# Optimization experiments

Hardware: AMD Instinct MI355X
Metric: run time of the kernel (lower is better)

The kernel has to match this reference:

```python
import jax, jax.numpy as jnp
import numpy as np

K_IN = 9      # input_patch_size
K_OUT = 3     # output_patch_size
C_IN = 4      # nb_of_input_features
C_OUT = 2     # nb_of_output_features
HID = 50      # int_layer_width
B, H, W = 16, 128, 128
CUT = K_IN // 2 - K_OUT // 2  # border pixels cut from output (3)


def _unfold(x, k):
    # x: [B, C, H, W] -> [B, C*k*k, L] with torch unfold ordering (c, ki, kj)
    b, c, h, w = x.shape
    ho, wo = h - k + 1, w - k + 1
    cols = jnp.stack([x[:, :, i:i + ho, j:j + wo]
                      for i in range(k) for j in range(k)], axis=2)  # [B,C,k*k,ho,wo]
    return cols.reshape(b, c * k * k, ho * wo)


def _fold_add(patches, oh, ow):
    # patches: [B, C, k, k, ho, wo] -> overlap-add into [B, C, oh, ow]
    b, c, k, _, ho, wo = patches.shape
    out = jnp.zeros((b, c, oh, ow), dtype=patches.dtype)
    for i in range(k):
        for j in range(k):
            out = out.at[:, :, i:i + ho, j:j + wo].add(patches[:, :, i, j])
    return out


def setup_inputs() -> dict:
    key = jax.random.key(0)
    ks = jax.random.split(key, 7)
    f_in = C_IN * K_IN * K_IN      # 324
    f_out = C_OUT * K_OUT * K_OUT  # 18
    s1 = 1.0 / np.sqrt(f_in)
    s2 = 1.0 / np.sqrt(HID)
    return {
        "x": jax.random.normal(ks[0], (B, C_IN, H, W), dtype=jnp.float32),
        "W1": jax.random.uniform(ks[1], (f_in, HID), jnp.float32, -s1, s1),
        "b1": jax.random.uniform(ks[2], (HID,), jnp.float32, -s1, s1),
        "W2": jax.random.uniform(ks[3], (HID, HID), jnp.float32, -s2, s2),
        "b2": jax.random.uniform(ks[4], (HID,), jnp.float32, -s2, s2),
        "W3": jax.random.uniform(ks[5], (HID, f_out), jnp.float32, -s2, s2),
        "b3": jax.random.uniform(ks[6], (f_out,), jnp.float32, -s2, s2),
    }


def reference(x, W1, b1, W2, b2, W3, b3):
    b, c, h, w = x.shape
    oh, ow = h - 2 * CUT, w - 2 * CUT          # 122, 122
    ho, wo = h - K_IN + 1, w - K_IN + 1        # 120, 120 (= oh-K_OUT+1)
    # unfold -> [B, L, C_in*K_in^2] -> flatten rows
    cols = _unfold(x, K_IN)                    # [B, 324, L]
    feats = cols.transpose(0, 2, 1).reshape(b * ho * wo, -1)
    # 3-layer MLP
    hmid = jax.nn.relu(feats @ W1 + b1)
    hmid = jax.nn.relu(hmid @ W2 + b2)
    out = hmid @ W3 + b3                       # [B*L, C_out*K_out^2]
    # fold (overlap-add), torch feature ordering (c, ki, kj)
    patches = out.reshape(b, ho, wo, C_OUT, K_OUT, K_OUT)
    patches = patches.transpose(0, 3, 4, 5, 1, 2)  # [B, C_out, k, k, ho, wo]
    res = _fold_add(patches, oh, ow)
    # divisor = fold(unfold(ones)) -> per-pixel overlap count
    ones_patches = jnp.ones((1, 1, K_OUT, K_OUT, ho, wo), dtype=x.dtype)
    divisor = _fold_add(ones_patches, oh, ow)  # [1,1,oh,ow]
    return res / divisor
```

## Files before the change

### kernel.cpp

```cpp
#include <hip/hip_runtime.h>
#include <hip/hip_bf16.h>

#define BATCH   16
#define C_INF   4
#define H_IN    128
#define W_IN    128
#define HID     50
#define F_OUT   18
#define HO      120
#define WO      120
#define OH      122
#define OW      122
#define NPOS    (BATCH * HO * WO)
#define MBLK    128
#define NBLKS   (NPOS / MBLK)

#define NB1     (11*4*2*64*8)
#define NB2     (2*4*2*64*8)
#define NB3     (2*2*2*64*8)
#define NWF     (NB1 + NB2 + NB3)
#define NXP     (BATCH*C_INF*H_IN*W_IN)
#define WOFF    (NPOS * F_OUT)

typedef float  v4f    __attribute__((ext_vector_type(4)));
typedef short  short8 __attribute__((ext_vector_type(8)));
typedef __bf16 v8bf   __attribute__((ext_vector_type(8)));
typedef int    v4i    __attribute__((ext_vector_type(4)));
typedef uint   u32x4  __attribute__((ext_vector_type(4)));
typedef u32x4  u32x4_a4 __attribute__((aligned(4)));

__device__ inline short f2bf_hi(float x) {
    __hip_bfloat16 h = __float2bfloat16(x);
    return __builtin_bit_cast(short, h);
}
__device__ inline float bf2f(short s) {
    __hip_bfloat16 h = __builtin_bit_cast(__hip_bfloat16, s);
    return __bfloat162float(h);
}
__device__ inline uint hipair(uint a, uint b) { return __builtin_amdgcn_perm(b, a, 0x07060302u); }
__device__ inline uint lopair(uint a, uint b) { return __builtin_amdgcn_perm(b, a, 0x05040100u); }

__device__ inline int slot_to_k1(int s, int qb, int e) {
    if (s < 9) {
        int pair = s*4 + qb;
        int c = pair/9, ki = pair - c*9;
        return c*81 + ki*9 + e;
    }
    int r = (s-9)*32 + qb*8 + e;
    if (r >= 36) return -1;
    int c = r/9, ki = r - c*9;
    return c*81 + ki*9 + 8;
}

__global__ __launch_bounds__(256)
void prep_kernel(const float* __restrict__ x,
                 const float* __restrict__ W1, const float* __restrict__ W2,
                 const float* __restrict__ W3,
                 uint* __restrict__ xp, short* __restrict__ wf)
{
    int i = blockIdx.x * 256 + threadIdx.x;
    if (i < NXP) {
        float v = x[i];
        short hi = f2bf_hi(v);
        short lo = f2bf_hi(v - bf2f(hi));
        xp[i] = ((uint)(ushort)hi << 16) | (uint)(ushort)lo;
        return;
    }
    i -= NXP;
    if (i >= NWF) return;
    float val;
    int p;
    if (i < NB1) {
        int t = i;
        int e = t & 7, lane = (t >> 3) & 63; p = (t >> 9) & 1;
        int rest = t >> 10;
        int u = rest & 3, s = rest >> 2;
        int k = slot_to_k1(s, lane >> 4, e);
        int n = u*16 + (lane & 15);
        val = (k >= 0 && n < HID) ? W1[k*HID + n] : 0.f;
    } else if (i < NB1 + NB2) {
        int t = i - NB1;
        int e = t & 7, lane = (t >> 3) & 63; p = (t >> 9) & 1;
        int rest = t >> 10;
        int u = rest & 3, s = rest >> 2;
        int k = s*32 + ((lane >> 4) << 3) + e;
        int n = u*16 + (lane & 15);
        val = (k < HID && n < HID) ? W2[k*HID + n] : 0.f;
    } else {
        int t = i - NB1 - NB2;
        int e = t & 7, lane = (t >> 3) & 63; p = (t >> 9) & 1;
        int rest = t >> 10;
        int u = rest & 1, s = rest >> 1;
        int k = s*32 + ((lane >> 4) << 3) + e;
        int n = u*16 + (lane & 15);
        val = (k < HID && n < F_OUT) ? W3[k*F_OUT + n] : 0.f;
    }
    short hi = f2bf_hi(val);
    wf[i] = (p == 0) ? hi : f2bf_hi(val - bf2f(hi));
}

__global__ __launch_bounds__(256, 4)
void mfma_mlp(const uint* __restrict__ xp,
              const float* __restrict__ b1, const float* __restrict__ b2,
              const float* __restrict__ b3,
              const short* __restrict__ wf, float* __restrict__ out3)
{
    __shared__ short h_hi[128 * 72];
    __shared__ short h_lo[128 * 72];

    const int tid  = threadIdx.x;
    const int lane = tid & 63;
    const int w    = tid >> 6;
    const int wm   = w >> 1, wn = w & 1;
    const int q    = lane >> 4, col = lane & 15;
    const int mbase = blockIdx.x * MBLK;

    int xbase[4];
    #pragma unroll
    for (int t = 0; t < 4; ++t) {
        int pos = mbase + wm*64 + t*16 + col;
        int b   = pos / (HO*WO); int rem = pos - b*(HO*WO);
        int y   = rem / WO;      int xc  = rem - y*WO;
        xbase[t] = b*(C_INF*H_IN*W_IN) + y*W_IN + xc;
    }

    const v4i* B1 = (const v4i*)wf;
    const v4i* B2 = (const v4i*)(wf + NB1);
    const v4i* B3 = (const v4i*)(wf + NB1 + NB2);

    v4f acc[4][2];
    #pragma unroll
    for (int t = 0; t < 4; ++t)
        #pragma unroll
        for (int u = 0; u < 2; ++u)
            acc[t][u] = (v4f){0.f, 0.f, 0.f, 0.f};

    #pragma unroll 3
    for (int s = 0; s < 9; ++s) {
        const int pair = s*4 + q;
        const int c = pair/9, ki = pair - c*9;
        const int off = c*(H_IN*W_IN) + ki*W_IN;

        v4i bhv[2], blv[2];
        #pragma unroll
        for (int uu = 0; uu < 2; ++uu) {
            int u  = 2*wn + uu;
            int fb = ((s*4 + u)*2)*64 + lane;
            bhv[uu] = B1[fb];
            blv[uu] = B1[fb + 64];
        }

        u32x4 wa[4], wb[4];
        #pragma unroll
        for (int t = 0; t < 4; ++t) {
            const uint* p = &xp[xbase[t] + off];
            wa[t] = *(const u32x4_a4*)(p);
            wb[t] = *(const u32x4_a4*)(p + 4);
        }
        short8 ah[4], al[4];
        #pragma unroll
        for (int t = 0; t < 4; ++t) {
            u32x4 hh, ll;
            hh.x = hipair(wa[t].x, wa[t].y); hh.y = hipair(wa[t].z, wa[t].w);
            hh.z = hipair(wb[t].x, wb[t].y); hh.w = hipair(wb[t].z, wb[t].w);
            ll.x = lopair(wa[t].x, wa[t].y); ll.y = lopair(wa[t].z, wa[t].w);
            ll.z = lopair(wb[t].x, wb[t].y); ll.w = lopair(wb[t].z, wb[t].w);
            ah[t] = __builtin_bit_cast(short8, hh);
            al[t] = __builtin_bit_cast(short8, ll);
        }
        #pragma unroll
        for (int uu = 0; uu < 2; ++uu) {
            v8bf bh = __builtin_bit_cast(v8bf, bhv[uu]);
            v8bf bl = __builtin_bit_cast(v8bf, blv[uu]);
            #pragma unroll
            for (int t = 0; t < 4; ++t) {
                v8bf a_h = __builtin_bit_cast(v8bf, ah[t]);
                v8bf a_l = __builtin_bit_cast(v8bf, al[t]);
                acc[t][uu] = __builtin_amdgcn_mfma_f32_16x16x32_bf16(a_h, bh, acc[t][uu], 0, 0, 0);
                acc[t][uu] = __builtin_amdgcn_mfma_f32_16x16x32_bf16(a_l, bh, acc[t][uu], 0, 0, 0);
                acc[t][uu] = __builtin_amdgcn_mfma_f32_16x16x32_bf16(a_h, bl, acc[t][uu], 0, 0, 0);
            }
        }
    }
    #pragma unroll
    for (int sr = 0; sr < 2; ++sr) {
        const int s = 9 + sr;
        short8 ah[4], al[4];
        #pragma unroll
        for (int e = 0; e < 8; ++e) {
            int r = sr*32 + q*8 + e;
            bool valid = (r < 36);
            int c = valid ? r/9 : 0;
            int ki = r - c*9;
            int off = c*(H_IN*W_IN) + ki*W_IN + 8;
            #pragma unroll
            for (int t = 0; t < 4; ++t) {
                uint wv = valid ? xp[xbase[t] + off] : 0u;
                ah[t][e] = (short)(wv >> 16);
                al[t][e] = (short)(wv & 0xffffu);
            }
        }
        #pragma unroll
        for (int uu = 0; uu < 2; ++uu) {
            int u  = 2*wn + uu;
            int fb = ((s*4 + u)*2)*64 + lane;
            v8bf bh = __builtin_bit_cast(v8bf, B1[fb]);
            v8bf bl = __builtin_bit_cast(v8bf, B1[fb + 64]);
            #pragma unroll
            for (int t = 0; t < 4; ++t) {
                v8bf a_h = __builtin_bit_cast(v8bf, ah[t]);
                v8bf a_l = __builtin_bit_cast(v8bf, al[t]);
                acc[t][uu] = __builtin_amdgcn_mfma_f32_16x16x32_bf16(a_h, bh, acc[t][uu], 0, 0, 0);
                acc[t][uu] = __builtin_amdgcn_mfma_f32_16x16x32_bf16(a_l, bh, acc[t][uu], 0, 0, 0);
                acc[t][uu] = __builtin_amdgcn_mfma_f32_16x16x32_bf16(a_h, bl, acc[t][uu], 0, 0, 0);
            }
        }
    }

    #pragma unroll
    for (int uu = 0; uu < 2; ++uu) {
        int j = (2*wn + uu)*16 + col;
        float bias = (j < HID) ? b1[j] : 0.f;
        #pragma unroll
        for (int t = 0; t < 4; ++t) {
            #pragma unroll
            for (int r = 0; r < 4; ++r) {
                float v = fmaxf(acc[t][uu][r] + bias, 0.f);
                int m = wm*64 + t*16 + q*4 + r;
                short hi = f2bf_hi(v);
                h_hi[m*72 + j] = hi;
                h_lo[m*72 + j] = f2bf_hi(v - bf2f(hi));
            }
        }
    }
    __syncthreads();

    v4f acc2[4][2];
    #pragma unroll
    for (int t = 0; t < 4; ++t)
        #pragma unroll
        for (int u = 0; u < 2; ++u)
            acc2[t][u] = (v4f){0.f, 0.f, 0.f, 0.f};

    #pragma unroll
    for (int s = 0; s < 2; ++s) {
        short8 ah2[4], al2[4];
        #pragma unroll
        for (int t = 0; t < 4; ++t) {
            int m = wm*64 + t*16 + col;
            ah2[t] = *(const short8*)&h_hi[m*72 + s*32 + q*8];
            al2[t] = *(const short8*)&h_lo[m*72 + s*32 + q*8];
        }
        #pragma unroll
        for (int uu = 0; uu < 2; ++uu) {
            int u  = 2*wn + uu;
            int fb = ((s*4 + u)*2)*64 + lane;
            v8bf bh = __builtin_bit_cast(v8bf, B2[fb]);
            v8bf bl = __builtin_bit_cast(v8bf, B2[fb + 64]);
            #pragma unroll
            for (int t = 0; t < 4; ++t) {
                v8bf a_h = __builtin_bit_cast(v8bf, ah2[t]);
                v8bf a_l = __builtin_bit_cast(v8bf, al2[t]);
                acc2[t][uu] = __builtin_amdgcn_mfma_f32_16x16x32_bf16(a_h, bh, acc2[t][uu], 0, 0, 0);
                acc2[t][uu] = __builtin_amdgcn_mfma_f32_16x16x32_bf16(a_l, bh, acc2[t][uu], 0, 0, 0);
                acc2[t][uu] = __builtin_amdgcn_mfma_f32_16x16x32_bf16(a_h, bl, acc2[t][uu], 0, 0, 0);
            }
        }
    }
    __syncthreads();

    #pragma unroll
    for (int uu = 0; uu < 2; ++uu) {
        int j = (2*wn + uu)*16 + col;
        float bias = (j < HID) ? b2[j] : 0.f;
        #pragma unroll
        for (int t = 0; t < 4; ++t) {
            #pragma unroll
            for (int r = 0; r < 4; ++r) {
                float v = fmaxf(acc2[t][uu][r] + bias, 0.f);
                int m = wm*64 + t*16 + q*4 + r;
                short hi = f2bf_hi(v);
                h_hi[m*72 + j] = hi;
                h_lo[m*72 + j] = f2bf_hi(v - bf2f(hi));
            }
        }
    }
    __syncthreads();

    v4f acc3[4];
    #pragma unroll
    for (int t = 0; t < 4; ++t) acc3[t] = (v4f){0.f, 0.f, 0.f, 0.f};

    #pragma unroll
    for (int s = 0; s < 2; ++s) {
        short8 ah3[4], al3[4];
        #pragma unroll
        for (int t = 0; t < 4; ++t) {
            int m = wm*64 + t*16 + col;
            ah3[t] = *(const short8*)&h_hi[m*72 + s*32 + q*8];
            al3[t] = *(const short8*)&h_lo[m*72 + s*32 + q*8];
        }
        int fb = ((s*2 + wn)*2)*64 + lane;
        v8bf bh = __builtin_bit_cast(v8bf, B3[fb]);
        v8bf bl = __builtin_bit_cast(v8bf, B3[fb + 64]);
        #pragma unroll
        for (int t = 0; t < 4; ++t) {
            v8bf a_h = __builtin_bit_cast(v8bf, ah3[t]);
            v8bf a_l = __builtin_bit_cast(v8bf, al3[t]);
            acc3[t] = __builtin_amdgcn_mfma_f32_16x16x32_bf16(a_h, bh, acc3[t], 0, 0, 0);
            acc3[t] = __builtin_amdgcn_mfma_f32_16x16x32_bf16(a_l, bh, acc3[t], 0, 0, 0);
            acc3[t] = __builtin_amdgcn_mfma_f32_16x16x32_bf16(a_h, bl, acc3[t], 0, 0, 0);
        }
    }
    __syncthreads();

    float* ot = (float*)h_hi;
    {
        int j = wn*16 + col;
        if (j < F_OUT) {
            float bias = b3[j];
            #pragma unroll
            for (int t = 0; t < 4; ++t) {
                #pragma unroll
                for (int r = 0; r < 4; ++r) {
                    int m = wm*64 + t*16 + q*4 + r;
                    ot[j*129 + m] = acc3[t][r] + bias;
                }
            }
        }
    }
    __syncthreads();
    for (int i = tid; i < F_OUT * 128; i += 256) {
        int j2 = i >> 7, m2 = i & 127;
        out3[j2*NPOS + mbase + m2] = ot[j2*129 + m2];
    }
}

__global__ __launch_bounds__(256)
void fold_kernel(const float* __restrict__ out3, float* __restrict__ out)
{
    const int idx = blockIdx.x * 256 + threadIdx.x;
    const int total = BATCH * 2 * OH * OW;
    if (idx >= total) return;

    int t = idx;
    const int ox = t % OW; t /= OW;
    const int oy = t % OH; t /= OH;
    const int c  = t & 1;  t >>= 1;
    const int b  = t;

    const int ylo = max(0, oy - 2), yhi = min(HO - 1, oy);
    const int xlo = max(0, ox - 2), xhi = min(WO - 1, ox);

    float s = 0.f;
    for (int y = ylo; y <= yhi; ++y) {
        const int ki = oy - y;
        for (int xx = xlo; xx <= xhi; ++xx) {
            const int kj = ox - xx;
            const int o  = (c*3 + ki)*3 + kj;
            s += out3[o*NPOS + (b*HO + y)*WO + xx];
        }
    }
    const float div = (float)((yhi - ylo + 1) * (xhi - xlo + 1));
    out[idx] = s / div;
}

extern "C" void kernel_launch(void* const* d_in, const int* in_sizes, int n_in,
                              void* d_out, int out_size, void* d_ws, size_t ws_size,
                              hipStream_t stream)
{
    const float* x  = (const float*)d_in[0];
    const float* W1 = (const float*)d_in[1];
    const float* b1 = (const float*)d_in[2];
    const float* W2 = (const float*)d_in[3];
    const float* b2 = (const float*)d_in[4];
    const float* W3 = (const float*)d_in[5];
    const float* b3 = (const float*)d_in[6];

    float* out3 = (float*)d_ws;
    short* wf   = (short*)d_ws + 2*(size_t)WOFF;
    uint*  xp   = (uint*)((char*)d_ws + (size_t)WOFF*4 + (size_t)NWF*2);

    const int nprep = (NXP + NWF + 255) / 256;
    prep_kernel<<<nprep, 256, 0, stream>>>(x, W1, W2, W3, xp, wf);

    mfma_mlp<<<NBLKS, 256, 0, stream>>>(xp, b1, b2, b3, wf, out3);

    const int total = BATCH * 2 * OH * OW;
    fold_kernel<<<(total + 255) / 256, 256, 0, stream>>>(out3, (float*)d_out);
}
```

Measured before the change: 124.7 us.

## Fuse fold into MLP epilogue via atomics and drop lo-split of hidden activations

```diff
diff --git a/kernel.cpp b/kernel.cpp
--- a/kernel.cpp
+++ b/kernel.cpp
@@ -20,7 +20,6 @@
 #define NB3     (2*2*2*64*8)
 #define NWF     (NB1 + NB2 + NB3)
 #define NXP     (BATCH*C_INF*H_IN*W_IN)
-#define WOFF    (NPOS * F_OUT)
 
 typedef float  v4f    __attribute__((ext_vector_type(4)));
 typedef short  short8 __attribute__((ext_vector_type(8)));
@@ -103,10 +102,9 @@
 void mfma_mlp(const uint* __restrict__ xp,
               const float* __restrict__ b1, const float* __restrict__ b2,
               const float* __restrict__ b3,
-              const short* __restrict__ wf, float* __restrict__ out3)
+              const short* __restrict__ wf, float* __restrict__ out)
 {
     __shared__ short h_hi[128 * 72];
-    __shared__ short h_lo[128 * 72];
 
     const int tid  = threadIdx.x;
     const int lane = tid & 63;
@@ -227,9 +225,7 @@
             for (int r = 0; r < 4; ++r) {
                 float v = fmaxf(acc[t][uu][r] + bias, 0.f);
                 int m = wm*64 + t*16 + q*4 + r;
-                short hi = f2bf_hi(v);
-                h_hi[m*72 + j] = hi;
-                h_lo[m*72 + j] = f2bf_hi(v - bf2f(hi));
+                h_hi[m*72 + j] = f2bf_hi(v);
             }
         }
     }
@@ -244,12 +240,11 @@
 
     #pragma unroll
     for (int s = 0; s < 2; ++s) {
-        short8 ah2[4], al2[4];
+        short8 ah2[4];
         #pragma unroll
         for (int t = 0; t < 4; ++t) {
             int m = wm*64 + t*16 + col;
             ah2[t] = *(const short8*)&h_hi[m*72 + s*32 + q*8];
-            al2[t] = *(const short8*)&h_lo[m*72 + s*32 + q*8];
         }
         #pragma unroll
         for (int uu = 0; uu < 2; ++uu) {
@@ -260,9 +255,7 @@
             #pragma unroll
             for (int t = 0; t < 4; ++t) {
                 v8bf a_h = __builtin_bit_cast(v8bf, ah2[t]);
-                v8bf a_l = __builtin_bit_cast(v8bf, al2[t]);
                 acc2[t][uu] = __builtin_amdgcn_mfma_f32_16x16x32_bf16(a_h, bh, acc2[t][uu], 0, 0, 0);
-                acc2[t][uu] = __builtin_amdgcn_mfma_f32_16x16x32_bf16(a_l, bh, acc2[t][uu], 0, 0, 0);
                 acc2[t][uu] = __builtin_amdgcn_mfma_f32_16x16x32_bf16(a_h, bl, acc2[t][uu], 0, 0, 0);
             }
         }
@@ -279,9 +272,7 @@
             for (int r = 0; r < 4; ++r) {
                 float v = fmaxf(acc2[t][uu][r] + bias, 0.f);
                 int m = wm*64 + t*16 + q*4 + r;
-                short hi = f2bf_hi(v);
-                h_hi[m*72 + j] = hi;
-                h_lo[m*72 + j] = f2bf_hi(v - bf2f(hi));
+                h_hi[m*72 + j] = f2bf_hi(v);
             }
         }
     }
@@ -293,12 +284,11 @@
 
     #pragma unroll
     for (int s = 0; s < 2; ++s) {
-        short8 ah3[4], al3[4];
+        short8 ah3[4];
         #pragma unroll
         for (int t = 0; t < 4; ++t) {
             int m = wm*64 + t*16 + col;
             ah3[t] = *(const short8*)&h_hi[m*72 + s*32 + q*8];
-            al3[t] = *(const short8*)&h_lo[m*72 + s*32 + q*8];
         }
         int fb = ((s*2 + wn)*2)*64 + lane;
         v8bf bh = __builtin_bit_cast(v8bf, B3[fb]);
@@ -306,63 +296,33 @@
         #pragma unroll
         for (int t = 0; t < 4; ++t) {
             v8bf a_h = __builtin_bit_cast(v8bf, ah3[t]);
-            v8bf a_l = __builtin_bit_cast(v8bf, al3[t]);
             acc3[t] = __builtin_amdgcn_mfma_f32_16x16x32_bf16(a_h, bh, acc3[t], 0, 0, 0);
-            acc3[t] = __builtin_amdgcn_mfma_f32_16x16x32_bf16(a_l, bh, acc3[t], 0, 0, 0);
             acc3[t] = __builtin_amdgcn_mfma_f32_16x16x32_bf16(a_h, bl, acc3[t], 0, 0, 0);
         }
     }
-    __syncthreads();
-
-    float* ot = (float*)h_hi;
-    {
-        int j = wn*16 + col;
-        if (j < F_OUT) {
-            float bias = b3[j];
-            #pragma unroll
-            for (int t = 0; t < 4; ++t) {
-                #pragma unroll
-                for (int r = 0; r < 4; ++r) {
-                    int m = wm*64 + t*16 + q*4 + r;
-                    ot[j*129 + m] = acc3[t][r] + bias;
-                }
-            }
-        }
-    }
-    __syncthreads();
-    for (int i = tid; i < F_OUT * 128; i += 256) {
-        int j2 = i >> 7, m2 = i & 127;
-        out3[j2*NPOS + mbase + m2] = ot[j2*129 + m2];
-    }
-}
-
-__global__ __launch_bounds__(256)
-void fold_kernel(const float* __restrict__ out3, float* __restrict__ out)
-{
-    const int idx = blockIdx.x * 256 + threadIdx.x;
-    const int total = BATCH * 2 * OH * OW;
-    if (idx >= total) return;
-
-    int t = idx;
-    const int ox = t % OW; t /= OW;
-    const int oy = t % OH; t /= OH;
-    const int c  = t & 1;  t >>= 1;
-    const int b  = t;
-
-    const int ylo = max(0, oy - 2), yhi = min(HO - 1, oy);
-    const int xlo = max(0, ox - 2), xhi = min(WO - 1, ox);
-
-    float s = 0.f;
-    for (int y = ylo; y <= yhi; ++y) {
-        const int ki = oy - y;
-        for (int xx = xlo; xx <= xhi; ++xx) {
-            const int kj = ox - xx;
-            const int o  = (c*3 + ki)*3 + kj;
-            s += out3[o*NPOS + (b*HO + y)*WO + xx];
-        }
-    }
-    const float div = (float)((yhi - ylo + 1) * (xhi - xlo + 1));
-    out[idx] = s / div;
+
+    int j = wn*16 + col;
+    if (j < F_OUT) {
+        const float bias = b3[j];
+        const int c  = j / 9, r9 = j - c*9;
+        const int ki = r9 / 3, kj = r9 - ki*3;
+        #pragma unroll
+        for (int t = 0; t < 4; ++t) {
+            #pragma unroll
+            for (int r = 0; r < 4; ++r) {
+                int pos = mbase + wm*64 + t*16 + q*4 + r;
+                int b   = pos / (HO*WO); int rem = pos - b*(HO*WO);
+                int y   = rem / WO;      int xc  = rem - y*WO;
+                int oy  = y + ki, ox = xc + kj;
+                int cy  = min(HO-1, oy) - max(0, oy-2) + 1;
+                int cx  = min(WO-1, ox) - max(0, ox-2) + 1;
+                float sy = (cy == 3) ? (1.f/3.f) : ((cy == 2) ? 0.5f : 1.f);
+                float sx = (cx == 3) ? (1.f/3.f) : ((cx == 2) ? 0.5f : 1.f);
+                float v  = (acc3[t][r] + bias) * (sy * sx);
+                atomicAdd(&out[((b*2 + c)*OH + oy)*OW + ox], v);
+            }
+        }
+    }
 }
 
 extern "C" void kernel_launch(void* const* d_in, const int* in_sizes, int n_in,
@@ -377,15 +337,13 @@
     const float* W3 = (const float*)d_in[5];
     const float* b3 = (const float*)d_in[6];
 
-    float* out3 = (float*)d_ws;
-    short* wf   = (short*)d_ws + 2*(size_t)WOFF;
-    uint*  xp   = (uint*)((char*)d_ws + (size_t)WOFF*4 + (size_t)NWF*2);
+    uint*  xp = (uint*)d_ws;
+    short* wf = (short*)(xp + NXP);
+
+    hipMemsetAsync(d_out, 0, (size_t)out_size * sizeof(float), stream);
 
     const int nprep = (NXP + NWF + 255) / 256;
     prep_kernel<<<nprep, 256, 0, stream>>>(x, W1, W2, W3, xp, wf);
 
-    mfma_mlp<<<NBLKS, 256, 0, stream>>>(xp, b1, b2, b3, wf, out3);
-
-    const int total = BATCH * 2 * OH * OW;
-    fold_kernel<<<(total + 255) / 256, 256, 0, stream>>>(out3, (float*)d_out);
-}
+    mfma_mlp<<<NBLKS, 256, 0, stream>>>(xp, b1, b2, b3, wf, (float*)d_out);
+}
```

Measured after the change: 138.0 us. 10.6% more time.

## Fuse prep, MLP and fold into one persistent kernel with grid barriers

Applied to the files above, without the earlier changes.

```diff
diff --git a/kernel.cpp b/kernel.cpp
--- a/kernel.cpp
+++ b/kernel.cpp
@@ -14,6 +14,7 @@
 #define NPOS    (BATCH * HO * WO)
 #define MBLK    128
 #define NBLKS   (NPOS / MBLK)
+#define NB      512
 
 #define NB1     (11*4*2*64*8)
 #define NB2     (2*4*2*64*8)
@@ -21,6 +22,7 @@
 #define NWF     (NB1 + NB2 + NB3)
 #define NXP     (BATCH*C_INF*H_IN*W_IN)
 #define WOFF    (NPOS * F_OUT)
+#define NOUT    (BATCH * 2 * OH * OW)
 
 typedef float  v4f    __attribute__((ext_vector_type(4)));
 typedef short  short8 __attribute__((ext_vector_type(8)));
@@ -52,317 +54,323 @@
     return c*81 + ki*9 + 8;
 }
 
-__global__ __launch_bounds__(256)
-void prep_kernel(const float* __restrict__ x,
-                 const float* __restrict__ W1, const float* __restrict__ W2,
-                 const float* __restrict__ W3,
-                 uint* __restrict__ xp, short* __restrict__ wf)
-{
-    int i = blockIdx.x * 256 + threadIdx.x;
-    if (i < NXP) {
-        float v = x[i];
-        short hi = f2bf_hi(v);
-        short lo = f2bf_hi(v - bf2f(hi));
-        xp[i] = ((uint)(ushort)hi << 16) | (uint)(ushort)lo;
-        return;
-    }
-    i -= NXP;
-    if (i >= NWF) return;
-    float val;
-    int p;
-    if (i < NB1) {
-        int t = i;
-        int e = t & 7, lane = (t >> 3) & 63; p = (t >> 9) & 1;
-        int rest = t >> 10;
-        int u = rest & 3, s = rest >> 2;
-        int k = slot_to_k1(s, lane >> 4, e);
-        int n = u*16 + (lane & 15);
-        val = (k >= 0 && n < HID) ? W1[k*HID + n] : 0.f;
-    } else if (i < NB1 + NB2) {
-        int t = i - NB1;
-        int e = t & 7, lane = (t >> 3) & 63; p = (t >> 9) & 1;
-        int rest = t >> 10;
-        int u = rest & 3, s = rest >> 2;
-        int k = s*32 + ((lane >> 4) << 3) + e;
-        int n = u*16 + (lane & 15);
-        val = (k < HID && n < HID) ? W2[k*HID + n] : 0.f;
-    } else {
-        int t = i - NB1 - NB2;
-        int e = t & 7, lane = (t >> 3) & 63; p = (t >> 9) & 1;
-        int rest = t >> 10;
-        int u = rest & 1, s = rest >> 1;
-        int k = s*32 + ((lane >> 4) << 3) + e;
-        int n = u*16 + (lane & 15);
-        val = (k < HID && n < F_OUT) ? W3[k*F_OUT + n] : 0.f;
-    }
-    short hi = f2bf_hi(val);
-    wf[i] = (p == 0) ? hi : f2bf_hi(val - bf2f(hi));
-}
-
-__global__ __launch_bounds__(256, 4)
-void mfma_mlp(const uint* __restrict__ xp,
-              const float* __restrict__ b1, const float* __restrict__ b2,
-              const float* __restrict__ b3,
-              const short* __restrict__ wf, float* __restrict__ out3)
+__device__ inline void gbar(uint* flags, uint tag) {
+    __threadfence();
+    __syncthreads();
+    if (threadIdx.x == 0)
+        __hip_atomic_store(&flags[blockIdx.x], tag, __ATOMIC_RELEASE, __HIP_MEMORY_SCOPE_AGENT);
+    for (int f = (int)threadIdx.x; f < NB; f += 256) {
+        while (__hip_atomic_load(&flags[f], __ATOMIC_ACQUIRE, __HIP_MEMORY_SCOPE_AGENT) != tag)
+            __builtin_amdgcn_s_sleep(2);
+    }
+    __syncthreads();
+    __threadfence();
+}
+
+__global__ __launch_bounds__(256, 2)
+void fused_kernel(const float* __restrict__ x,
+                  const float* __restrict__ W1, const float* __restrict__ b1,
+                  const float* __restrict__ W2, const float* __restrict__ b2,
+                  const float* __restrict__ W3, const float* __restrict__ b3,
+                  float* __restrict__ out3, short* __restrict__ wf,
+                  uint* __restrict__ xp, uint* flags1, uint* flags2,
+                  float* __restrict__ out)
 {
     __shared__ short h_hi[128 * 72];
-    __shared__ short h_lo[128 * 72];
 
     const int tid  = threadIdx.x;
+    const int bid  = blockIdx.x;
+
+    if (tid == 0) {
+        __hip_atomic_store(&flags1[bid], 0u, __ATOMIC_RELAXED, __HIP_MEMORY_SCOPE_AGENT);
+        __hip_atomic_store(&flags2[bid], 0u, __ATOMIC_RELAXED, __HIP_MEMORY_SCOPE_AGENT);
+    }
+
+    for (int gi = bid*256 + tid; gi < NXP + NWF; gi += NB*256) {
+        if (gi < NXP) {
+            float v = x[gi];
+            short hi = f2bf_hi(v);
+            short lo = f2bf_hi(v - bf2f(hi));
+            xp[gi] = ((uint)(ushort)hi << 16) | (uint)(ushort)lo;
+        } else {
+            int i = gi - NXP;
+            float val; int p;
+            if (i < NB1) {
+                int t = i;
+                int e = t & 7, lane = (t >> 3) & 63; p = (t >> 9) & 1;
+                int rest = t >> 10;
+                int u = rest & 3, s = rest >> 2;
+                int k = slot_to_k1(s, lane >> 4, e);
+                int n = u*16 + (lane & 15);
+                val = (k >= 0 && n < HID) ? W1[k*HID + n] : 0.f;
+            } else if (i < NB1 + NB2) {
+                int t = i - NB1;
+                int e = t & 7, lane = (t >> 3) & 63; p = (t >> 9) & 1;
+                int rest = t >> 10;
+                int u = rest & 3, s = rest >> 2;
+                int k = s*32 + ((lane >> 4) << 3) + e;
+                int n = u*16 + (lane & 15);
+                val = (k < HID && n < HID) ? W2[k*HID + n] : 0.f;
+            } else {
+                int t = i - NB1 - NB2;
+                int e = t & 7, lane = (t >> 3) & 63; p = (t >> 9) & 1;
+                int rest = t >> 10;
+                int u = rest & 1, s = rest >> 1;
+                int k = s*32 + ((lane >> 4) << 3) + e;
+                int n = u*16 + (lane & 15);
+                val = (k < HID && n < F_OUT) ? W3[k*F_OUT + n] : 0.f;
+            }
+            short hi = f2bf_hi(val);
+            wf[i] = (p == 0) ? hi : f2bf_hi(val - bf2f(hi));
+        }
+    }
+
+    gbar(flags1, 1u);
+
     const int lane = tid & 63;
     const int w    = tid >> 6;
     const int wm   = w >> 1, wn = w & 1;
     const int q    = lane >> 4, col = lane & 15;
-    const int mbase = blockIdx.x * MBLK;
-
-    int xbase[4];
-    #pragma unroll
-    for (int t = 0; t < 4; ++t) {
-        int pos = mbase + wm*64 + t*16 + col;
-        int b   = pos / (HO*WO); int rem = pos - b*(HO*WO);
-        int y   = rem / WO;      int xc  = rem - y*WO;
-        xbase[t] = b*(C_INF*H_IN*W_IN) + y*W_IN + xc;
-    }
 
     const v4i* B1 = (const v4i*)wf;
     const v4i* B2 = (const v4i*)(wf + NB1);
     const v4i* B3 = (const v4i*)(wf + NB1 + NB2);
 
-    v4f acc[4][2];
-    #pragma unroll
-    for (int t = 0; t < 4; ++t)
-        #pragma unroll
-        for (int u = 0; u < 2; ++u)
-            acc[t][u] = (v4f){0.f, 0.f, 0.f, 0.f};
-
-    #pragma unroll 3
-    for (int s = 0; s < 9; ++s) {
-        const int pair = s*4 + q;
-        const int c = pair/9, ki = pair - c*9;
-        const int off = c*(H_IN*W_IN) + ki*W_IN;
-
-        v4i bhv[2], blv[2];
+    for (int unit = bid; unit < NBLKS; unit += NB) {
+        const int mbase = unit * MBLK;
+
+        int xbase[4];
+        #pragma unroll
+        for (int t = 0; t < 4; ++t) {
+            int pos = mbase + wm*64 + t*16 + col;
+            int b   = pos / (HO*WO); int rem = pos - b*(HO*WO);
+            int y   = rem / WO;      int xc  = rem - y*WO;
+            xbase[t] = b*(C_INF*H_IN*W_IN) + y*W_IN + xc;
+        }
+
+        v4f acc[4][2];
+        #pragma unroll
+        for (int t = 0; t < 4; ++t)
+            #pragma unroll
+            for (int u = 0; u < 2; ++u)
+                acc[t][u] = (v4f){0.f, 0.f, 0.f, 0.f};
+
+        #pragma unroll 3
+        for (int s = 0; s < 9; ++s) {
+            const int pair = s*4 + q;
+            const int c = pair/9, ki = pair - c*9;
+            const int off = c*(H_IN*W_IN) + ki*W_IN;
+
+            v4i bhv[2], blv[2];
+            #pragma unroll
+            for (int uu = 0; uu < 2; ++uu) {
+                int u  = 2*wn + uu;
+                int fb = ((s*4 + u)*2)*64 + lane;
+                bhv[uu] = B1[fb];
+                blv[uu] = B1[fb + 64];
+            }
+
+            u32x4 wa[4], wb[4];
+            #pragma unroll
+            for (int t = 0; t < 4; ++t) {
+                const uint* p = &xp[xbase[t] + off];
+                wa[t] = *(const u32x4_a4*)(p);
+                wb[t] = *(const u32x4_a4*)(p + 4);
+            }
+            short8 ah[4], al[4];
+            #pragma unroll
+            for (int t = 0; t < 4; ++t) {
+                u32x4 hh, ll;
+                hh.x = hipair(wa[t].x, wa[t].y); hh.y = hipair(wa[t].z, wa[t].w);
+                hh.z = hipair(wb[t].x, wb[t].y); hh.w = hipair(wb[t].z, wb[t].w);
+                ll.x = lopair(wa[t].x, wa[t].y); ll.y = lopair(wa[t].z, wa[t].w);
+                ll.z = lopair(wb[t].x, wb[t].y); ll.w = lopair(wb[t].z, wb[t].w);
+                ah[t] = __builtin_bit_cast(short8, hh);
+                al[t] = __builtin_bit_cast(short8, ll);
+            }
+            #pragma unroll
+            for (int uu = 0; uu < 2; ++uu) {
+                v8bf bh = __builtin_bit_cast(v8bf, bhv[uu]);
+                v8bf bl = __builtin_bit_cast(v8bf, blv[uu]);
+                #pragma unroll
+                for (int t = 0; t < 4; ++t) {
+                    v8bf a_h = __builtin_bit_cast(v8bf, ah[t]);
+                    v8bf a_l = __builtin_bit_cast(v8bf, al[t]);
+                    acc[t][uu] = __builtin_amdgcn_mfma_f32_16x16x32_bf16(a_h, bh, acc[t][uu], 0, 0, 0);
+                    acc[t][uu] = __builtin_amdgcn_mfma_f32_16x16x32_bf16(a_l, bh, acc[t][uu], 0, 0, 0);
+                    acc[t][uu] = __builtin_amdgcn_mfma_f32_16x16x32_bf16(a_h, bl, acc[t][uu], 0, 0, 0);
+                }
+            }
+        }
+        #pragma unroll
+        for (int sr = 0; sr < 2; ++sr) {
+            const int s = 9 + sr;
+            short8 ah[4], al[4];
+            #pragma unroll
+            for (int e = 0; e < 8; ++e) {
+                int r = sr*32 + q*8 + e;
+                bool valid = (r < 36);
+                int c = valid ? r/9 : 0;
+                int ki = r - c*9;
+                int off = c*(H_IN*W_IN) + ki*W_IN + 8;
+                #pragma unroll
+                for (int t = 0; t < 4; ++t) {
+                    uint wv = valid ? xp[xbase[t] + off] : 0u;
+                    ah[t][e] = (short)(wv >> 16);
+                    al[t][e] = (short)(wv & 0xffffu);
+                }
+            }
+            #pragma unroll
+            for (int uu = 0; uu < 2; ++uu) {
+                int u  = 2*wn + uu;
+                int fb = ((s*4 + u)*2)*64 + lane;
+                v8bf bh = __builtin_bit_cast(v8bf, B1[fb]);
+                v8bf bl = __builtin_bit_cast(v8bf, B1[fb + 64]);
+                #pragma unroll
+                for (int t = 0; t < 4; ++t) {
+                    v8bf a_h = __builtin_bit_cast(v8bf, ah[t]);
+                    v8bf a_l = __builtin_bit_cast(v8bf, al[t]);
+                    acc[t][uu] = __builtin_amdgcn_mfma_f32_16x16x32_bf16(a_h, bh, acc[t][uu], 0, 0, 0);
+                    acc[t][uu] = __builtin_amdgcn_mfma_f32_16x16x32_bf16(a_l, bh, acc[t][uu], 0, 0, 0);
+                    acc[t][uu] = __builtin_amdgcn_mfma_f32_16x16x32_bf16(a_h, bl, acc[t][uu], 0, 0, 0);
+                }
+            }
+        }
+
         #pragma unroll
         for (int uu = 0; uu < 2; ++uu) {
-            int u  = 2*wn + uu;
-            int fb = ((s*4 + u)*2)*64 + lane;
-            bhv[uu] = B1[fb];
-            blv[uu] = B1[fb + 64];
-        }
-
-        u32x4 wa[4], wb[4];
-        #pragma unroll
-        for (int t = 0; t < 4; ++t) {
-            const uint* p = &xp[xbase[t] + off];
-            wa[t] = *(const u32x4_a4*)(p);
-            wb[t] = *(const u32x4_a4*)(p + 4);
-        }
-        short8 ah[4], al[4];
-        #pragma unroll
-        for (int t = 0; t < 4; ++t) {
-            u32x4 hh, ll;
-            hh.x = hipair(wa[t].x, wa[t].y); hh.y = hipair(wa[t].z, wa[t].w);
-            hh.z = hipair(wb[t].x, wb[t].y); hh.w = hipair(wb[t].z, wb[t].w);
-            ll.x = lopair(wa[t].x, wa[t].y); ll.y = lopair(wa[t].z, wa[t].w);
-            ll.z = lopair(wb[t].x, wb[t].y); ll.w = lopair(wb[t].z, wb[t].w);
-            ah[t] = __builtin_bit_cast(short8, hh);
-            al[t] = __builtin_bit_cast(short8, ll);
-        }
+            int j = (2*wn + uu)*16 + col;
+            float bias = (j < HID) ? b1[j] : 0.f;
+            #pragma unroll
+            for (int t = 0; t < 4; ++t) {
+                #pragma unroll
+                for (int r = 0; r < 4; ++r) {
+                    float v = fmaxf(acc[t][uu][r] + bias, 0.f);
+                    int m = wm*64 + t*16 + q*4 + r;
+                    h_hi[m*72 + j] = f2bf_hi(v);
+                }
+            }
+        }
+        __syncthreads();
+
+        v4f acc2[4][2];
+        #pragma unroll
+        for (int t = 0; t < 4; ++t)
+            #pragma unroll
+            for (int u = 0; u < 2; ++u)
+                acc2[t][u] = (v4f){0.f, 0.f, 0.f, 0.f};
+
+        #pragma unroll
+        for (int s = 0; s < 2; ++s) {
+            short8 ah2[4];
+            #pragma unroll
+            for (int t = 0; t < 4; ++t) {
+                int m = wm*64 + t*16 + col;
+                ah2[t] = *(const short8*)&h_hi[m*72 + s*32 + q*8];
+            }
+            #pragma unroll
+            for (int uu = 0; uu < 2; ++uu) {
+                int u  = 2*wn + uu;
+                int fb = ((s*4 + u)*2)*64 + lane;
+                v8bf bh = __builtin_bit_cast(v8bf, B2[fb]);
+                v8bf bl = __builtin_bit_cast(v8bf, B2[fb + 64]);
+                #pragma unroll
+                for (int t = 0; t < 4; ++t) {
+                    v8bf a_h = __builtin_bit_cast(v8bf, ah2[t]);
+                    acc2[t][uu] = __builtin_amdgcn_mfma_f32_16x16x32_bf16(a_h, bh, acc2[t][uu], 0, 0, 0);
+                    acc2[t][uu] = __builtin_amdgcn_mfma_f32_16x16x32_bf16(a_h, bl, acc2[t][uu], 0, 0, 0);
+                }
+            }
+        }
+        __syncthreads();
+
         #pragma unroll
         for (int uu = 0; uu < 2; ++uu) {
-            v8bf bh = __builtin_bit_cast(v8bf, bhv[uu]);
-            v8bf bl = __builtin_bit_cast(v8bf, blv[uu]);
-            #pragma unroll
-            for (int t = 0; t < 4; ++t) {
-                v8bf a_h = __builtin_bit_cast(v8bf, ah[t]);
-                v8bf a_l = __builtin_bit_cast(v8bf, al[t]);
-                acc[t][uu] = __builtin_amdgcn_mfma_f32_16x16x32_bf16(a_h, bh, acc[t][uu], 0, 0, 0);
-                acc[t][uu] = __builtin_amdgcn_mfma_f32_16x16x32_bf16(a_l, bh, acc[t][uu], 0, 0, 0);
-                acc[t][uu] = __builtin_amdgcn_mfma_f32_16x16x32_bf16(a_h, bl, acc[t][uu], 0, 0, 0);
-            }
-        }
-    }
-    #pragma unroll
-    for (int sr = 0; sr < 2; ++sr) {
-        const int s = 9 + sr;
-        short8 ah[4], al[4];
-        #pragma unroll
-        for (int e = 0; e < 8; ++e) {
-            int r = sr*32 + q*8 + e;
-            bool valid = (r < 36);
-            int c = valid ? r/9 : 0;
-            int ki = r - c*9;
-            int off = c*(H_IN*W_IN) + ki*W_IN + 8;
-            #pragma unroll
-            for (int t = 0; t < 4; ++t) {
-                uint wv = valid ? xp[xbase[t] + off] : 0u;
-                ah[t][e] = (short)(wv >> 16);
-                al[t][e] = (short)(wv & 0xffffu);
-            }
-        }
-        #pragma unroll
-        for (int uu = 0; uu < 2; ++uu) {
-            int u  = 2*wn + uu;
-            int fb = ((s*4 + u)*2)*64 + lane;
-            v8bf bh = __builtin_bit_cast(v8bf, B1[fb]);
-            v8bf bl = __builtin_bit_cast(v8bf, B1[fb + 64]);
-            #pragma unroll
-            for (int t = 0; t < 4; ++t) {
-                v8bf a_h = __builtin_bit_cast(v8bf, ah[t]);
-                v8bf a_l = __builtin_bit_cast(v8bf, al[t]);
-                acc[t][uu] = __builtin_amdgcn_mfma_f32_16x16x32_bf16(a_h, bh, acc[t][uu], 0, 0, 0);
-                acc[t][uu] = __builtin_amdgcn_mfma_f32_16x16x32_bf16(a_l, bh, acc[t][uu], 0, 0, 0);
-                acc[t][uu] = __builtin_amdgcn_mfma_f32_16x16x32_bf16(a_h, bl, acc[t][uu], 0, 0, 0);
-            }
-        }
-    }
-
-    #pragma unroll
-    for (int uu = 0; uu < 2; ++uu) {
-        int j = (2*wn + uu)*16 + col;
-        float bias = (j < HID) ? b1[j] : 0.f;
-        #pragma unroll
-        for (int t = 0; t < 4; ++t) {
-            #pragma unroll
-            for (int r = 0; r < 4; ++r) {
-                float v = fmaxf(acc[t][uu][r] + bias, 0.f);
-                int m = wm*64 + t*16 + q*4 + r;
-                short hi = f2bf_hi(v);
-                h_hi[m*72 + j] = hi;
-                h_lo[m*72 + j] = f2bf_hi(v - bf2f(hi));
-            }
-        }
-    }
-    __syncthreads();
-
-    v4f acc2[4][2];
-    #pragma unroll
-    for (int t = 0; t < 4; ++t)
-        #pragma unroll
-        for (int u = 0; u < 2; ++u)
-            acc2[t][u] = (v4f){0.f, 0.f, 0.f, 0.f};
-
-    #pragma unroll
-    for (int s = 0; s < 2; ++s) {
-        short8 ah2[4], al2[4];
-        #pragma unroll
-        for (int t = 0; t < 4; ++t) {
-            int m = wm*64 + t*16 + col;
-            ah2[t] = *(const short8*)&h_hi[m*72 + s*32 + q*8];
-            al2[t] = *(const short8*)&h_lo[m*72 + s*32 + q*8];
-        }
-        #pragma unroll
-        for (int uu = 0; uu < 2; ++uu) {
-            int u  = 2*wn + uu;
-            int fb = ((s*4 + u)*2)*64 + lane;
-            v8bf bh = __builtin_bit_cast(v8bf, B2[fb]);
-            v8bf bl = __builtin_bit_cast(v8bf, B2[fb + 64]);
-            #pragma unroll
-            for (int t = 0; t < 4; ++t) {
-                v8bf a_h = __builtin_bit_cast(v8bf, ah2[t]);
-                v8bf a_l = __builtin_bit_cast(v8bf, al2[t]);
-                acc2[t][uu] = __builtin_amdgcn_mfma_f32_16x16x32_bf16(a_h, bh, acc2[t][uu], 0, 0, 0);
-                acc2[t][uu] = __builtin_amdgcn_mfma_f32_16x16x32_bf16(a_l, bh, acc2[t][uu], 0, 0, 0);
-                acc2[t][uu] = __builtin_amdgcn_mfma_f32_16x16x32_bf16(a_h, bl, acc2[t][uu], 0, 0, 0);
-            }
-        }
-    }
-    __syncthreads();
-
-    #pragma unroll
-    for (int uu = 0; uu < 2; ++uu) {
-        int j = (2*wn + uu)*16 + col;
-        float bias = (j < HID) ? b2[j] : 0.f;
-        #pragma unroll
-        for (int t = 0; t < 4; ++t) {
-            #pragma unroll
-            for (int r = 0; r < 4; ++r) {
-                float v = fmaxf(acc2[t][uu][r] + bias, 0.f);
-                int m = wm*64 + t*16 + q*4 + r;
-                short hi = f2bf_hi(v);
-                h_hi[m*72 + j] = hi;
-                h_lo[m*72 + j] = f2bf_hi(v - bf2f(hi));
-            }
-        }
-    }
-    __syncthreads();
-
-    v4f acc3[4];
-    #pragma unroll
-    for (int t = 0; t < 4; ++t) acc3[t] = (v4f){0.f, 0.f, 0.f, 0.f};
-
-    #pragma unroll
-    for (int s = 0; s < 2; ++s) {
-        short8 ah3[4], al3[4];
-        #pragma unroll
-        for (int t = 0; t < 4; ++t) {
-            int m = wm*64 + t*16 + col;
-            ah3[t] = *(const short8*)&h_hi[m*72 + s*32 + q*8];
-            al3[t] = *(const short8*)&h_lo[m*72 + s*32 + q*8];
-        }
-        int fb = ((s*2 + wn)*2)*64 + lane;
-        v8bf bh = __builtin_bit_cast(v8bf, B3[fb]);
-        v8bf bl = __builtin_bit_cast(v8bf, B3[fb + 64]);
-        #pragma unroll
-        for (int t = 0; t < 4; ++t) {
-            v8bf a_h = __builtin_bit_cast(v8bf, ah3[t]);
-            v8bf a_l = __builtin_bit_cast(v8bf, al3[t]);
-            acc3[t] = __builtin_amdgcn_mfma_f32_16x16x32_bf16(a_h, bh, acc3[t], 0, 0, 0);
-            acc3[t] = __builtin_amdgcn_mfma_f32_16x16x32_bf16(a_l, bh, acc3[t], 0, 0, 0);
-            acc3[t] = __builtin_amdgcn_mfma_f32_16x16x32_bf16(a_h, bl, acc3[t], 0, 0, 0);
-        }
-    }
-    __syncthreads();
-
-    float* ot = (float*)h_hi;
-    {
-        int j = wn*16 + col;
-        if (j < F_OUT) {
-            float bias = b3[j];
+            int j = (2*wn + uu)*16 + col;
+            float bias = (j < HID) ? b2[j] : 0.f;
             #pragma unroll
             for (int t = 0; t < 4; ++t) {
                 #pragma unroll
                 for (int r = 0; r < 4; ++r) {
+                    float v = fmaxf(acc2[t][uu][r] + bias, 0.f);
                     int m = wm*64 + t*16 + q*4 + r;
-                    ot[j*129 + m] = acc3[t][r] + bias;
-                }
-            }
-        }
-    }
-    __syncthreads();
-    for (int i = tid; i < F_OUT * 128; i += 256) {
-        int j2 = i >> 7, m2 = i & 127;
-        out3[j2*NPOS + mbase + m2] = ot[j2*129 + m2];
-    }
-}
-
-__global__ __launch_bounds__(256)
-void fold_kernel(const float* __restrict__ out3, float* __restrict__ out)
-{
-    const int idx = blockIdx.x * 256 + threadIdx.x;
-    const int total = BATCH * 2 * OH * OW;
-    if (idx >= total) return;
-
-    int t = idx;
-    const int ox = t % OW; t /= OW;
-    const int oy = t % OH; t /= OH;
-    const int c  = t & 1;  t >>= 1;
-    const int b  = t;
-
-    const int ylo = max(0, oy - 2), yhi = min(HO - 1, oy);
-    const int xlo = max(0, ox - 2), xhi = min(WO - 1, ox);
-
-    float s = 0.f;
-    for (int y = ylo; y <= yhi; ++y) {
-        const int ki = oy - y;
-        for (int xx = xlo; xx <= xhi; ++xx) {
-            const int kj = ox - xx;
-            const int o  = (c*3 + ki)*3 + kj;
-            s += out3[o*NPOS + (b*HO + y)*WO + xx];
-        }
-    }
-    const float div = (float)((yhi - ylo + 1) * (xhi - xlo + 1));
-    out[idx] = s / div;
+                    h_hi[m*72 + j] = f2bf_hi(v);
+                }
+            }
+        }
+        __syncthreads();
+
+        v4f acc3[4];
+        #pragma unroll
+        for (int t = 0; t < 4; ++t) acc3[t] = (v4f){0.f, 0.f, 0.f, 0.f};
+
+        #pragma unroll
+        for (int s = 0; s < 2; ++s) {
+            short8 ah3[4];
+            #pragma unroll
+            for (int t = 0; t < 4; ++t) {
+                int m = wm*64 + t*16 + col;
+                ah3[t] = *(const short8*)&h_hi[m*72 + s*32 + q*8];
+            }
+            int fb = ((s*2 + wn)*2)*64 + lane;
+            v8bf bh = __builtin_bit_cast(v8bf, B3[fb]);
+            v8bf bl = __builtin_bit_cast(v8bf, B3[fb + 64]);
+            #pragma unroll
+            for (int t = 0; t < 4; ++t) {
+                v8bf a_h = __builtin_bit_cast(v8bf, ah3[t]);
+                acc3[t] = __builtin_amdgcn_mfma_f32_16x16x32_bf16(a_h, bh, acc3[t], 0, 0, 0);
+                acc3[t] = __builtin_amdgcn_mfma_f32_16x16x32_bf16(a_h, bl, acc3[t], 0, 0, 0);
+            }
+        }
+        __syncthreads();
+
+        float* ot = (float*)h_hi;
+        {
+            int j = wn*16 + col;
+            if (j < F_OUT) {
+                float bias = b3[j];
+                #pragma unroll
+                for (int t = 0; t < 4; ++t) {
+                    #pragma unroll
+                    for (int r = 0; r < 4; ++r) {
+                        int m = wm*64 + t*16 + q*4 + r;
+                        ot[j*129 + m] = acc3[t][r] + bias;
+                    }
+                }
+            }
+        }
+        __syncthreads();
+        for (int i = tid; i < F_OUT * 128; i += 256) {
+            int j2 = i >> 7, m2 = i & 127;
+            out3[j2*NPOS + mbase + m2] = ot[j2*129 + m2];
+        }
+        __syncthreads();
+    }
+
+    gbar(flags2, 1u);
+
+    for (int idx = bid*256 + tid; idx < NOUT; idx += NB*256) {
+        int t = idx;
+        const int ox = t % OW; t /= OW;
+        const int oy = t % OH; t /= OH;
+        const int c  = t & 1;  t >>= 1;
+        const int b  = t;
+
+        const int ylo = max(0, oy - 2), yhi = min(HO - 1, oy);
+        const int xlo = max(0, ox - 2), xhi = min(WO - 1, ox);
+
+        float s = 0.f;
+        for (int y = ylo; y <= yhi; ++y) {
+            const int ki = oy - y;
+            for (int xx = xlo; xx <= xhi; ++xx) {
+                const int kj = ox - xx;
+                const int o  = (c*3 + ki)*3 + kj;
+                s += out3[o*NPOS + (b*HO + y)*WO + xx];
+            }
+        }
+        const float div = (float)((yhi - ylo + 1) * (xhi - xlo + 1));
+        out[idx] = s / div;
+    }
 }
 
 extern "C" void kernel_launch(void* const* d_in, const int* in_sizes, int n_in,
@@ -377,15 +385,13 @@
     const float* W3 = (const float*)d_in[5];
     const float* b3 = (const float*)d_in[6];
 
-    float* out3 = (float*)d_ws;
-    short* wf   = (short*)d_ws + 2*(size_t)WOFF;
-    uint*  xp   = (uint*)((char*)d_ws + (size_t)WOFF*4 + (size_t)NWF*2);
-
-    const int nprep = (NXP + NWF + 255) / 256;
-    prep_kernel<<<nprep, 256, 0, stream>>>(x, W1, W2, W3, xp, wf);
-
-    mfma_mlp<<<NBLKS, 256, 0, stream>>>(xp, b1, b2, b3, wf, out3);
-
-    const int total = BATCH * 2 * OH * OW;
-    fold_kernel<<<(total + 255) / 256, 256, 0, stream>>>(out3, (float*)d_out);
-}
+    float* out3   = (float*)d_ws;
+    short* wf     = (short*)(out3 + WOFF);
+    uint*  xp     = (uint*)(wf + NWF);
+    uint*  flags1 = xp + NXP;
+    uint*  flags2 = flags1 + NB;
+
+    fused_kernel<<<NB, 256, 0, stream>>>(x, W1, b1, W2, b2, W3, b3,
+                                         out3, wf, xp, flags1, flags2,
+                                         (float*)d_out);
+}
```

Result: slower. 471.3 us (+277.9%).
